# Kernel tuning notes

Hardware: AMD Instinct MI355X
Metric: run time of the kernel (lower is better)

The kernel has to match this reference:

```python
import jax, jax.numpy as jnp
import numpy as np

N = 50000        # nodes
E = 800000       # random edges (plus N self-loops added in setup)
DIN = 128        # input_dim
H = 128          # hidden_dim
L = 3            # num_layers
EPS = 1e-5       # BatchNorm1d eps


def _bn(x, gamma, beta):
    # BatchNorm1d in training mode: batch stats over node axis, biased variance
    m = x.mean(axis=0)
    v = jnp.mean((x - m) ** 2, axis=0)
    return (x - m) * jax.lax.rsqrt(v + EPS) * gamma + beta


def setup_inputs() -> dict:
    key = jax.random.key(0)
    ks = jax.random.split(key, 11)
    feats = jax.random.normal(ks[0], (N, DIN), dtype=jnp.float32)
    # edge list with self-loops so every node has degree >= 1 (average pooling divides by degree)
    loops = jnp.arange(N, dtype=jnp.int64)
    src = jnp.concatenate([jax.random.randint(ks[1], (E,), 0, N, dtype=jnp.int64), loops])
    dst = jnp.concatenate([jax.random.randint(ks[2], (E,), 0, N, dtype=jnp.int64), loops])
    s = 0.05
    # per-layer MLP params (num_mlp_layers=2: Linear -> BN -> ReLU -> Linear), layer 0 has DIN==H
    W1 = jax.random.normal(ks[3], (L, DIN, H), dtype=jnp.float32) * s
    b1 = jnp.zeros((L, H), jnp.float32)
    g1 = jnp.ones((L, H), jnp.float32)
    be1 = jnp.zeros((L, H), jnp.float32)
    W2 = jax.random.normal(ks[4], (L, H, H), dtype=jnp.float32) * s
    b2 = jnp.zeros((L, H), jnp.float32)
    # outer BatchNorm1d per GNN layer
    og = jnp.ones((L, H), jnp.float32)
    ob = jnp.zeros((L, H), jnp.float32)
    return {"feats": feats, "W1": W1, "b1": b1, "g1": g1, "be1": be1,
            "W2": W2, "b2": b2, "og": og, "ob": ob, "src": src, "dst": dst}


def reference(feats, W1, b1, g1, be1, W2, b2, og, ob, src, dst):
    n = feats.shape[0]
    # degree = spmm(Adj, ones) -- constant across layers
    deg = jax.ops.segment_sum(jnp.ones(src.shape, jnp.float32), dst, num_segments=n)[:, None]
    h = feats
    for l in range(L):
        # pooled = spmm(Adj, h) via edge gather + segment reduce, then 'average' normalize
        pooled = jax.ops.segment_sum(h[src], dst, num_segments=n) / deg
        # GIN-style 2-layer MLP: Linear -> BN -> ReLU -> Linear
        z = jax.nn.relu(_bn(pooled @ W1[l] + b1[l], g1[l], be1[l]))
        z = z @ W2[l] + b2[l]
        # outer BatchNorm + ReLU
        h = jax.nn.relu(_bn(z, og[l], ob[l]))
    return h
```

## Files before the change

kernel.cpp:

```cpp
#include <hip/hip_runtime.h>
#include <hip/hip_bf16.h>
#include <stdint.h>

typedef _Float16 h16;
typedef h16 h16x2 __attribute__((ext_vector_type(2)));
typedef h16 h16x8 __attribute__((ext_vector_type(8)));
typedef float f32x4 __attribute__((ext_vector_type(4)));

#define HF 128
#define EPS 1e-5f
#define BSH 9
#define BROWS 512
#define BCAP 16384
#define ECHUNK 8192
#define SBANKS 8

union pk32 { uint32_t u; h16x2 h; };

static __device__ __forceinline__ uint32_t pack_h16(float a, float b) {
    pk32 c;
    c.h[0] = (h16)a; c.h[1] = (h16)b;
    return c.u;
}

static __device__ __forceinline__ float sum8(const float* __restrict__ st, int idx) {
    float s = 0.f;
#pragma unroll
    for (int b = 0; b < SBANKS; b++) s += st[b * 256 + idx];
    return s;
}


__global__ __launch_bounds__(256) void k_bscatter(const int* __restrict__ src,
                                                  const int* __restrict__ dst,
                                                  int* __restrict__ gcursor,
                                                  int2* __restrict__ staging, int ne, int nb) {
    __shared__ int h[128], gb[128];
    const int tid = threadIdx.x;
    if (tid < nb) h[tid] = 0;
    __syncthreads();
    const int beg = blockIdx.x * ECHUNK;
    const int end = min(beg + ECHUNK, ne);
    for (int i = beg + tid; i < end; i += 256)
        atomicAdd(&h[dst[i] >> BSH], 1);
    __syncthreads();
    if (tid < nb) {
        int c = h[tid];
        gb[tid] = c ? atomicAdd(&gcursor[tid], c) : 0;
        h[tid] = 0;
    }
    __syncthreads();
    for (int i = beg + tid; i < end; i += 256) {
        int d = dst[i];
        int b = d >> BSH;
        int r = atomicAdd(&h[b], 1);
        staging[(size_t)b * BCAP + gb[b] + r] = make_int2(src[i], d);
    }
}

__global__ __launch_bounds__(256) void k_bbuild(const int2* __restrict__ staging,
                                                const int* __restrict__ gcursor,
                                                int* __restrict__ rowbeg,
                                                int* __restrict__ rowend,
                                                float* __restrict__ deginv,
                                                int* __restrict__ csrsrc, int n) {
    __shared__ int hist[BROWS];
    __shared__ int scan[BROWS];
    const int b = blockIdx.x;
    const int tid = threadIdx.x;
    const int rb = b << BSH;
    const int nrows = min(BROWS, n - rb);
    const int base = b * BCAP;
    const int cnt = gcursor[b];
    hist[tid] = 0; hist[tid + 256] = 0;
    __syncthreads();
    for (int i = tid; i < cnt; i += 256)
        atomicAdd(&hist[staging[base + i].y - rb], 1);
    __syncthreads();
    const int i0 = tid, i1 = tid + 256;
    scan[i0] = hist[i0]; scan[i1] = hist[i1];
    __syncthreads();
    for (int off = 1; off < BROWS; off <<= 1) {
        int v0 = (i0 >= off) ? scan[i0 - off] : 0;
        int v1 = (i1 >= off) ? scan[i1 - off] : 0;
        __syncthreads();
        scan[i0] += v0; scan[i1] += v1;
        __syncthreads();
    }
    for (int r = tid; r < BROWS; r += 256) {
        int c = hist[r];
        int excl = scan[r] - c;
        if (r < nrows) {
            rowbeg[rb + r] = base + excl;
            rowend[rb + r] = base + excl + c;
            deginv[rb + r] = c ? 1.0f / (float)c : 0.f;
        }
        scan[r] = excl;
    }
    __syncthreads();
    for (int i = tid; i < cnt; i += 256) {
        int2 e = staging[base + i];
        int pos = atomicAdd(&scan[e.y - rb], 1);
        csrsrc[base + pos] = e.x;
    }
}

__global__ __launch_bounds__(256) void k_prep(const float* __restrict__ W1,
                                              const float* __restrict__ W2,
                                              h16* __restrict__ wp,
                                              const float* __restrict__ feats,
                                              uint32_t* __restrict__ hbuf, long tot2) {
    const int bid = (int)blockIdx.x;
    if (bid < 384) {
        const int mat = bid >> 6;
        const int idx = ((bid & 63) << 8) + (int)threadIdx.x;
        const int l = mat >> 1;
        const float* Wsrc = (mat & 1) ? (W2 + l * 16384) : (W1 + l * 16384);
        const int nn = idx >> 7, k = idx & 127;
        float w = Wsrc[k * 128 + nn];
        int pos = nn * 128 + ((((k >> 3) ^ (nn & 7))) << 3) + (k & 7);
        wp[mat * 16384 + pos] = (h16)w;
    } else {
        long i = (long)(bid - 384) * 256 + threadIdx.x;
        if (i < tot2) {
            float2 v = ((const float2*)feats)[i];
            hbuf[i] = pack_h16(v.x, v.y);
        }
    }
}

template <int AFF>
__global__ __launch_bounds__(256) void k_spmm(const uint32_t* __restrict__ hp,
                                              const int* __restrict__ rowbeg,
                                              const int* __restrict__ rowend,
                                              const float* __restrict__ deginv,
                                              const float* __restrict__ st,
                                              const float* __restrict__ g,
                                              const float* __restrict__ be,
                                              float inv_n,
                                              const int* __restrict__ csrsrc,
                                              uint32_t* __restrict__ pooled, int n, int np) {
    const int wid  = (int)((blockIdx.x * 256u + threadIdx.x) >> 6);
    const int lane = threadIdx.x & 63;
    if (wid >= np) return;
    const int gg = lane >> 4;
    const int fl = lane & 15;
    uint4* outrow = (uint4*)(pooled + (size_t)wid * 64);
    if (wid >= n) {
        if (gg == 0) outrow[fl] = make_uint4(0u, 0u, 0u, 0u);
        return;
    }

    uint32_t sv[4], cv[4];
    if (AFF) {
        const int c0 = lane * 2, c1 = c0 + 1;
        float m0 = sum8(st, c0) * inv_n, v0 = sum8(st, 128 + c0) * inv_n - m0 * m0;
        float sx = g[c0] * rsqrtf(v0 + EPS), cx = be[c0] - m0 * sx;
        float m1 = sum8(st, c1) * inv_n, v1 = sum8(st, 128 + c1) * inv_n - m1 * m1;
        float sy = g[c1] * rsqrtf(v1 + EPS), cy = be[c1] - m1 * sy;
        uint32_t su = pack_h16(sx, sy);
        uint32_t cu = pack_h16(cx, cy);
#pragma unroll
        for (int w = 0; w < 4; w++) {
            sv[w] = (uint32_t)__shfl((int)su, fl * 4 + w);
            cv[w] = (uint32_t)__shfl((int)cu, fl * 4 + w);
        }
    }

    const h16 z0 = (h16)0.f;
    h16x2 acc[4];
#pragma unroll
    for (int w = 0; w < 4; w++) acc[w] = (h16x2)z0;

    const int beg = rowbeg[wid], end = rowend[wid];
    for (int base = beg; base < end; base += 64) {
        const int rem = end - base;
        const int cnt = rem < 64 ? rem : 64;
        const int off = lane < cnt ? lane : cnt - 1;
        const int idx = csrsrc[base + off];
        for (int j = 0; j < cnt; j += 32) {
            uint4 p[8];
#pragma unroll
            for (int u = 0; u < 8; u++) {
                const int eb = j + u * 4;
                if (eb < cnt) {
                    int ge = eb + gg;
                    int gec = ge < cnt ? ge : cnt - 1;
                    int s = __shfl(idx, gec);
                    p[u] = *(const uint4*)(hp + (size_t)s * 64 + (fl << 2));
                }
            }
#pragma unroll
            for (int u = 0; u < 8; u++) {
                const int eb = j + u * 4;
                if (eb < cnt) {
                    const uint32_t* pw = (const uint32_t*)&p[u];
                    h16x2 v[4];
#pragma unroll
                    for (int w = 0; w < 4; w++) {
                        pk32 t; t.u = pw[w];
                        h16x2 x = t.h;
                        if (AFF) {
                            pk32 s2; s2.u = sv[w];
                            pk32 c2; c2.u = cv[w];
                            x = x * s2.h + c2.h;
                            x[0] = x[0] > z0 ? x[0] : z0;
                            x[1] = x[1] > z0 ? x[1] : z0;
                        }
                        v[w] = x;
                    }
                    if (eb + gg < cnt) {
#pragma unroll
                        for (int w = 0; w < 4; w++) acc[w] = acc[w] + v[w];
                    }
                }
            }
        }
    }

#pragma unroll
    for (int w = 0; w < 4; w++) {
        pk32 t; t.h = acc[w];
        pk32 r1; r1.u = (uint32_t)__shfl_xor((int)t.u, 16);
        t.h = t.h + r1.h;
        pk32 r2; r2.u = (uint32_t)__shfl_xor((int)t.u, 32);
        t.h = t.h + r2.h;
        acc[w] = t.h;
    }

    const float di = deginv[wid];
    uint4 o;
    o.x = pack_h16((float)acc[0][0] * di, (float)acc[0][1] * di);
    o.y = pack_h16((float)acc[1][0] * di, (float)acc[1][1] * di);
    o.z = pack_h16((float)acc[2][0] * di, (float)acc[2][1] * di);
    o.w = pack_h16((float)acc[3][0] * di, (float)acc[3][1] * di);
    if (gg == 0) outrow[fl] = o;
}

template <int MODE>
__global__ __launch_bounds__(256) void k_gemm(const uint32_t* __restrict__ Ap,
                                              const h16* __restrict__ Wp,
                                              const float* __restrict__ bias,
                                              const float* __restrict__ st,
                                              const float* __restrict__ g,
                                              const float* __restrict__ be,
                                              float inv_n,
                                              h16* __restrict__ Y,
                                              float* __restrict__ outstats, int n) {
    __shared__ __align__(16) h16 WT[128 * 128];
    __shared__ float sred[4][128];
    __shared__ float sred2[4][128];
    __shared__ float aff[256];
    const int tid = threadIdx.x;
    const int wave = tid >> 6, lane = tid & 63;

    {
        const char* gsrc = (const char*)Wp + wave * 1024 + lane * 16;
        char* ldst = (char*)&WT[0] + wave * 1024;
#pragma unroll
        for (int i = 0; i < 8; i++) {
            __builtin_amdgcn_global_load_lds(
                (const __attribute__((address_space(1))) uint32_t*)(gsrc + i * 4096),
                (__attribute__((address_space(3))) uint32_t*)(ldst + i * 4096),
                16, 0, 0);
        }
    }
    if (MODE == 1 && tid < 128) {
        float m = sum8(st, tid) * inv_n;
        float v = sum8(st, 128 + tid) * inv_n - m * m;
        float a = g[tid] * rsqrtf(v + EPS);
        aff[tid] = a;
        aff[128 + tid] = be[tid] - m * a;
    }

    const int lrow = lane & 15, quad = lane >> 4;
    const int bx = (int)blockIdx.x * 128;
    int mb[2];
    mb[0] = bx + wave * 16;
    mb[1] = bx + 64 + wave * 16;

    h16x8 ah[2][4];
    uint4 araw[2][4];
#pragma unroll
    for (int rt = 0; rt < 2; rt++) {
        const uint32_t* arow = Ap + (size_t)(mb[rt] + lrow) * 64 + quad * 4;
#pragma unroll
        for (int kt = 0; kt < 4; kt++)
            araw[rt][kt] = *(const uint4*)(arow + kt * 16);
    }

    __syncthreads();

#pragma unroll
    for (int rt = 0; rt < 2; rt++) {
#pragma unroll
        for (int kt = 0; kt < 4; kt++) {
            if (MODE == 0) {
                ah[rt][kt] = *(const h16x8*)&araw[rt][kt];
            } else {
                const uint32_t* pw = (const uint32_t*)&araw[rt][kt];
                h16x8 t;
#pragma unroll
                for (int j2 = 0; j2 < 4; j2++) {
                    pk32 w; w.u = pw[j2];
                    int k = kt * 32 + quad * 8 + j2 * 2;
                    float x0 = fmaxf(fmaf((float)w.h[0], aff[k],     aff[128 + k]),     0.f);
                    float x1 = fmaxf(fmaf((float)w.h[1], aff[k + 1], aff[129 + k]), 0.f);
                    t[2 * j2]     = (h16)x0;
                    t[2 * j2 + 1] = (h16)x1;
                }
                ah[rt][kt] = t;
            }
        }
    }

    f32x4 acc[2][8];
#pragma unroll
    for (int rt = 0; rt < 2; rt++)
#pragma unroll
        for (int nt = 0; nt < 8; nt++) acc[rt][nt] = (f32x4){0.f, 0.f, 0.f, 0.f};

    const int sw = lrow & 7;
#pragma unroll
    for (int nt = 0; nt < 8; nt++) {
        const h16* wbase = &WT[(nt * 16 + lrow) * 128];
#pragma unroll
        for (int kt = 0; kt < 4; kt++) {
            h16x8 bh = *(const h16x8*)(wbase + (((4 * kt + quad) ^ sw) << 3));
#pragma unroll
            for (int rt = 0; rt < 2; rt++)
                acc[rt][nt] = __builtin_amdgcn_mfma_f32_16x16x32_f16(ah[rt][kt], bh, acc[rt][nt], 0, 0, 0);
        }
    }

#pragma unroll
    for (int nt = 0; nt < 8; nt++) {
        int col = nt * 16 + lrow;
        float bv = bias[col];
        float csum = 0.f, csq = 0.f;
#pragma unroll
        for (int rt = 0; rt < 2; rt++) {
#pragma unroll
            for (int r = 0; r < 4; r++) {
                int row = mb[rt] + quad * 4 + r;
                float yv = acc[rt][nt][r] + bv;
                Y[(size_t)row * 128 + col] = (h16)yv;
                if (row < n) { csum += yv; csq += yv * yv; }
            }
        }
        csum += __shfl_xor(csum, 16, 64); csum += __shfl_xor(csum, 32, 64);
        csq  += __shfl_xor(csq,  16, 64); csq  += __shfl_xor(csq,  32, 64);
        if (quad == 0) { sred[wave][col] = csum; sred2[wave][col] = csq; }
    }
    __syncthreads();
    if (tid < 128) {
        float s = sred[0][tid] + sred[1][tid] + sred[2][tid] + sred[3][tid];
        float q = sred2[0][tid] + sred2[1][tid] + sred2[2][tid] + sred2[3][tid];
        const int bank = (int)(blockIdx.x & (SBANKS - 1));
        atomicAdd(&outstats[bank * 256 + tid], s);
        atomicAdd(&outstats[bank * 256 + 128 + tid], q);
    }
}

__global__ __launch_bounds__(256) void k_bnrelu(const uint32_t* __restrict__ Z,
                                                const float* __restrict__ st,
                                                const float* __restrict__ g,
                                                const float* __restrict__ be,
                                                float inv_n,
                                                float* __restrict__ out, long tot2) {
    long i = (long)blockIdx.x * 256 + threadIdx.x;
    if (i >= tot2) return;
    int c = (int)((i * 2) & 127);
    float m0 = sum8(st, c) * inv_n,     v0 = sum8(st, 128 + c) * inv_n - m0 * m0;
    float a0 = g[c] * rsqrtf(v0 + EPS),     c0 = be[c] - m0 * a0;
    float m1 = sum8(st, c + 1) * inv_n, v1 = sum8(st, 129 + c) * inv_n - m1 * m1;
    float a1 = g[c + 1] * rsqrtf(v1 + EPS), c1 = be[c + 1] - m1 * a1;
    pk32 w; w.u = Z[i];
    float2 o;
    o.x = fmaxf(fmaf((float)w.h[0], a0, c0), 0.f);
    o.y = fmaxf(fmaf((float)w.h[1], a1, c1), 0.f);
    ((float2*)out)[i] = o;
}

extern "C" void kernel_launch(void* const* d_in, const int* in_sizes, int n_in,
                              void* d_out, int out_size, void* d_ws, size_t ws_size,
                              hipStream_t stream) {
    const float* feats = (const float*)d_in[0];
    const float* W1    = (const float*)d_in[1];
    const float* b1    = (const float*)d_in[2];
    const float* g1    = (const float*)d_in[3];
    const float* be1   = (const float*)d_in[4];
    const float* W2    = (const float*)d_in[5];
    const float* b2    = (const float*)d_in[6];
    const float* og    = (const float*)d_in[7];
    const float* ob    = (const float*)d_in[8];
    const int*   src   = (const int*)d_in[9];
    const int*   dst   = (const int*)d_in[10];

    const int n  = in_sizes[0] / HF;
    const int ne = in_sizes[9];
    const int np = (n + 127) & ~127;
    const int nb = (n + BROWS - 1) >> BSH;

    char* p = (char*)d_ws;
    auto alloc = [&](size_t bytes) -> char* {
        char* r = p;
        p += (bytes + 511) & ~(size_t)511;
        return r;
    };
    uint32_t* hbuf    = (uint32_t*)alloc((size_t)np * 64 * 4);
    uint32_t* pooled  = (uint32_t*)alloc((size_t)np * 64 * 4);
    uint32_t* ybuf    = (uint32_t*)alloc((size_t)np * 64 * 4);
    uint32_t* zb      = (uint32_t*)alloc((size_t)np * 64 * 4);
    h16*      wprep   = (h16*)     alloc(6 * 16384 * 2);
    float*    deginv  = (float*)   alloc((size_t)n * 4);
    int*      rowbeg  = (int*)     alloc((size_t)n * 4);
    int*      rowend  = (int*)     alloc((size_t)n * 4);
    int*      csrsrc  = (int*)     alloc((size_t)nb * BCAP * 4);
    int2*     staging = (int2*)    alloc((size_t)nb * BCAP * 8);
    char*     zone    = alloc(512 + 6 * SBANKS * 256 * 4);
    int*      gcursor = (int*)zone;
    float*    stats6  = (float*)(zone + 512);

    hipMemsetAsync(zone, 0, 512 + 6 * SBANKS * 256 * 4, stream);

    const long tot2  = (long)n * (HF / 2);
    const int bnb    = (int)((tot2 + 255) / 256);
    const int spmmb  = np / 4;
    const int gemmb  = np / 128;
    const float inv_n = 1.0f / (float)n;
    const int ebk = (ne + ECHUNK - 1) / ECHUNK;
    const int SL = SBANKS * 256;

    k_prep    <<<384 + bnb, 256, 0, stream>>>(W1, W2, wprep, feats, hbuf, tot2);
    k_bscatter<<<ebk, 256, 0, stream>>>(src, dst, gcursor, staging, ne, nb);
    k_bbuild  <<<nb, 256, 0, stream>>>(staging, gcursor, rowbeg, rowend, deginv, csrsrc, n);

    for (int l = 0; l < 3; l++) {
        float* sY = stats6 + (2 * l) * SL;
        float* sZ = stats6 + (2 * l + 1) * SL;
        if (l == 0)
            k_spmm<0><<<spmmb, 256, 0, stream>>>(hbuf, rowbeg, rowend, deginv,
                                                 nullptr, nullptr, nullptr, inv_n,
                                                 csrsrc, pooled, n, np);
        else
            k_spmm<1><<<spmmb, 256, 0, stream>>>(zb, rowbeg, rowend, deginv,
                                                 stats6 + (2 * (l - 1) + 1) * SL,
                                                 og + (l - 1) * HF, ob + (l - 1) * HF, inv_n,
                                                 csrsrc, pooled, n, np);
        k_gemm<0><<<gemmb, 256, 0, stream>>>(pooled,
                                             wprep + (size_t)(2 * l) * 16384,
                                             b1 + l * HF,
                                             nullptr, nullptr, nullptr, inv_n,
                                             (h16*)ybuf, sY, n);
        k_gemm<1><<<gemmb, 256, 0, stream>>>(ybuf,
                                             wprep + (size_t)(2 * l + 1) * 16384,
                                             b2 + l * HF,
                                             sY, g1 + l * HF, be1 + l * HF, inv_n,
                                             (h16*)zb, sZ, n);
    }
    k_bnrelu<<<bnb, 256, 0, stream>>>(zb, stats6 + 5 * SL, og + 2 * HF, ob + 2 * HF,
                                      inv_n, (float*)d_out, tot2);
}
```

Before: 375.0 us.

## Fuse both MLP GEMMs and final BN-ReLU into one kernel with grid barriers

Merges the two per-layer GEMM kernels into a single kernel that keeps the first GEMM's output tile in LDS. It uses a software grid barrier so the BatchNorm statistics are complete before the second GEMM runs. On the last layer a second barrier lets the kernel apply the outer BN+ReLU directly and write fp32 output, which removes the separate bnrelu kernel. This avoids writing and re-reading the intermediate Y buffer and saves launches. The costs are that all 391 blocks must be co-resident for the barrier to work, and that doubling LDS use for weights can lower occupancy.

Measured after the change: 504.3 us. +34.5%, slower.

```diff
diff --git a/kernel.cpp b/kernel.cpp
--- a/kernel.cpp
+++ b/kernel.cpp
@@ -28,6 +28,26 @@
 #pragma unroll
     for (int b = 0; b < SBANKS; b++) s += st[b * 256 + idx];
     return s;
+}
+
+static __device__ __forceinline__ float sum8c(const float* st, int idx) {
+    float s = 0.f;
+#pragma unroll
+    for (int b = 0; b < SBANKS; b++)
+        s += __hip_atomic_load(&st[b * 256 + idx], __ATOMIC_RELAXED, __HIP_MEMORY_SCOPE_AGENT);
+    return s;
+}
+
+static __device__ __forceinline__ void gridbar(int* ctr, int nblk) {
+    __syncthreads();
+    if (threadIdx.x == 0) {
+        __threadfence();
+        __hip_atomic_fetch_add(ctr, 1, __ATOMIC_ACQ_REL, __HIP_MEMORY_SCOPE_AGENT);
+        while (__hip_atomic_load(ctr, __ATOMIC_ACQUIRE, __HIP_MEMORY_SCOPE_AGENT) < nblk)
+            __builtin_amdgcn_s_sleep(2);
+        __threadfence();
+    }
+    __syncthreads();
 }
 
 
@@ -237,17 +257,25 @@
     if (gg == 0) outrow[fl] = o;
 }
 
-template <int MODE>
-__global__ __launch_bounds__(256) void k_gemm(const uint32_t* __restrict__ Ap,
-                                              const h16* __restrict__ Wp,
-                                              const float* __restrict__ bias,
-                                              const float* __restrict__ st,
-                                              const float* __restrict__ g,
-                                              const float* __restrict__ be,
-                                              float inv_n,
-                                              h16* __restrict__ Y,
-                                              float* __restrict__ outstats, int n) {
-    __shared__ __align__(16) h16 WT[128 * 128];
+template <int LAST>
+__global__ __launch_bounds__(256, 2) void k_fused(const uint32_t* __restrict__ Ap,
+                                                  const h16* __restrict__ Wp1,
+                                                  const h16* __restrict__ Wp2,
+                                                  const float* __restrict__ bias1,
+                                                  const float* __restrict__ bias2,
+                                                  const float* __restrict__ gi,
+                                                  const float* __restrict__ bei,
+                                                  const float* __restrict__ go,
+                                                  const float* __restrict__ bo,
+                                                  float* __restrict__ stY,
+                                                  float* __restrict__ stZ,
+                                                  int* bar1, int* bar2,
+                                                  float inv_n,
+                                                  h16* __restrict__ Zout,
+                                                  float* __restrict__ Fout,
+                                                  int n, int nblk) {
+    __shared__ __align__(16) h16 WT1[128 * 128];
+    __shared__ __align__(16) h16 WT2[128 * 128];
     __shared__ float sred[4][128];
     __shared__ float sred2[4][128];
     __shared__ float aff[256];
@@ -255,35 +283,33 @@
     const int wave = tid >> 6, lane = tid & 63;
 
     {
-        const char* gsrc = (const char*)Wp + wave * 1024 + lane * 16;
-        char* ldst = (char*)&WT[0] + wave * 1024;
+        const char* g1p = (const char*)Wp1 + wave * 1024 + lane * 16;
+        char* l1p = (char*)&WT1[0] + wave * 1024;
+        const char* g2p = (const char*)Wp2 + wave * 1024 + lane * 16;
+        char* l2p = (char*)&WT2[0] + wave * 1024;
 #pragma unroll
         for (int i = 0; i < 8; i++) {
             __builtin_amdgcn_global_load_lds(
-                (const __attribute__((address_space(1))) uint32_t*)(gsrc + i * 4096),
-                (__attribute__((address_space(3))) uint32_t*)(ldst + i * 4096),
+                (const __attribute__((address_space(1))) uint32_t*)(g1p + i * 4096),
+                (__attribute__((address_space(3))) uint32_t*)(l1p + i * 4096),
                 16, 0, 0);
-        }
-    }
-    if (MODE == 1 && tid < 128) {
-        float m = sum8(st, tid) * inv_n;
-        float v = sum8(st, 128 + tid) * inv_n - m * m;
-        float a = g[tid] * rsqrtf(v + EPS);
-        aff[tid] = a;
-        aff[128 + tid] = be[tid] - m * a;
+            __builtin_amdgcn_global_load_lds(
+                (const __attribute__((address_space(1))) uint32_t*)(g2p + i * 4096),
+                (__attribute__((address_space(3))) uint32_t*)(l2p + i * 4096),
+                16, 0, 0);
+        }
     }
 
     const int lrow = lane & 15, quad = lane >> 4;
     const int bx = (int)blockIdx.x * 128;
     int mb[2];
-    mb[0] = bx + wave * 16;
-    mb[1] = bx + 64 + wave * 16;
-
-    h16x8 ah[2][4];
+    mb[0] = wave * 16;
+    mb[1] = 64 + wave * 16;
+
     uint4 araw[2][4];
 #pragma unroll
     for (int rt = 0; rt < 2; rt++) {
-        const uint32_t* arow = Ap + (size_t)(mb[rt] + lrow) * 64 + quad * 4;
+        const uint32_t* arow = Ap + (size_t)(bx + mb[rt] + lrow) * 64 + quad * 4;
 #pragma unroll
         for (int kt = 0; kt < 4; kt++)
             araw[rt][kt] = *(const uint4*)(arow + kt * 16);
@@ -291,29 +317,6 @@
 
     __syncthreads();
 
-#pragma unroll
-    for (int rt = 0; rt < 2; rt++) {
-#pragma unroll
-        for (int kt = 0; kt < 4; kt++) {
-            if (MODE == 0) {
-                ah[rt][kt] = *(const h16x8*)&araw[rt][kt];
-            } else {
-                const uint32_t* pw = (const uint32_t*)&araw[rt][kt];
-                h16x8 t;
-#pragma unroll
-                for (int j2 = 0; j2 < 4; j2++) {
-                    pk32 w; w.u = pw[j2];
-                    int k = kt * 32 + quad * 8 + j2 * 2;
-                    float x0 = fmaxf(fmaf((float)w.h[0], aff[k],     aff[128 + k]),     0.f);
-                    float x1 = fmaxf(fmaf((float)w.h[1], aff[k + 1], aff[129 + k]), 0.f);
-                    t[2 * j2]     = (h16)x0;
-                    t[2 * j2 + 1] = (h16)x1;
-                }
-                ah[rt][kt] = t;
-            }
-        }
-    }
-
     f32x4 acc[2][8];
 #pragma unroll
     for (int rt = 0; rt < 2; rt++)
@@ -323,29 +326,34 @@
     const int sw = lrow & 7;
 #pragma unroll
     for (int nt = 0; nt < 8; nt++) {
-        const h16* wbase = &WT[(nt * 16 + lrow) * 128];
+        const h16* wbase = &WT1[(nt * 16 + lrow) * 128];
 #pragma unroll
         for (int kt = 0; kt < 4; kt++) {
             h16x8 bh = *(const h16x8*)(wbase + (((4 * kt + quad) ^ sw) << 3));
 #pragma unroll
-            for (int rt = 0; rt < 2; rt++)
-                acc[rt][nt] = __builtin_amdgcn_mfma_f32_16x16x32_f16(ah[rt][kt], bh, acc[rt][nt], 0, 0, 0);
-        }
-    }
+            for (int rt = 0; rt < 2; rt++) {
+                h16x8 a = *(const h16x8*)&araw[rt][kt];
+                acc[rt][nt] = __builtin_amdgcn_mfma_f32_16x16x32_f16(a, bh, acc[rt][nt], 0, 0, 0);
+            }
+        }
+    }
+
+    __syncthreads();
 
 #pragma unroll
     for (int nt = 0; nt < 8; nt++) {
         int col = nt * 16 + lrow;
-        float bv = bias[col];
+        float bv = bias1[col];
         float csum = 0.f, csq = 0.f;
 #pragma unroll
         for (int rt = 0; rt < 2; rt++) {
 #pragma unroll
             for (int r = 0; r < 4; r++) {
-                int row = mb[rt] + quad * 4 + r;
+                int rloc = mb[rt] + quad * 4 + r;
                 float yv = acc[rt][nt][r] + bv;
-                Y[(size_t)row * 128 + col] = (h16)yv;
-                if (row < n) { csum += yv; csq += yv * yv; }
+                int byte = rloc * 256 + ((2 * col) ^ ((rloc & 7) << 4));
+                *(h16*)((char*)WT1 + byte) = (h16)yv;
+                if (bx + rloc < n) { csum += yv; csq += yv * yv; }
             }
         }
         csum += __shfl_xor(csum, 16, 64); csum += __shfl_xor(csum, 32, 64);
@@ -357,29 +365,111 @@
         float s = sred[0][tid] + sred[1][tid] + sred[2][tid] + sred[3][tid];
         float q = sred2[0][tid] + sred2[1][tid] + sred2[2][tid] + sred2[3][tid];
         const int bank = (int)(blockIdx.x & (SBANKS - 1));
-        atomicAdd(&outstats[bank * 256 + tid], s);
-        atomicAdd(&outstats[bank * 256 + 128 + tid], q);
-    }
-}
-
-__global__ __launch_bounds__(256) void k_bnrelu(const uint32_t* __restrict__ Z,
-                                                const float* __restrict__ st,
-                                                const float* __restrict__ g,
-                                                const float* __restrict__ be,
-                                                float inv_n,
-                                                float* __restrict__ out, long tot2) {
-    long i = (long)blockIdx.x * 256 + threadIdx.x;
-    if (i >= tot2) return;
-    int c = (int)((i * 2) & 127);
-    float m0 = sum8(st, c) * inv_n,     v0 = sum8(st, 128 + c) * inv_n - m0 * m0;
-    float a0 = g[c] * rsqrtf(v0 + EPS),     c0 = be[c] - m0 * a0;
-    float m1 = sum8(st, c + 1) * inv_n, v1 = sum8(st, 129 + c) * inv_n - m1 * m1;
-    float a1 = g[c + 1] * rsqrtf(v1 + EPS), c1 = be[c + 1] - m1 * a1;
-    pk32 w; w.u = Z[i];
-    float2 o;
-    o.x = fmaxf(fmaf((float)w.h[0], a0, c0), 0.f);
-    o.y = fmaxf(fmaf((float)w.h[1], a1, c1), 0.f);
-    ((float2*)out)[i] = o;
+        atomicAdd(&stY[bank * 256 + tid], s);
+        atomicAdd(&stY[bank * 256 + 128 + tid], q);
+    }
+
+    gridbar(bar1, nblk);
+
+    if (tid < 128) {
+        float m = sum8c(stY, tid) * inv_n;
+        float v = sum8c(stY, 128 + tid) * inv_n - m * m;
+        float a = gi[tid] * rsqrtf(v + EPS);
+        aff[tid] = a;
+        aff[128 + tid] = bei[tid] - m * a;
+    }
+    __syncthreads();
+
+    h16x8 ah2[2][4];
+#pragma unroll
+    for (int rt = 0; rt < 2; rt++) {
+#pragma unroll
+        for (int kt = 0; kt < 4; kt++) {
+            int rloc = mb[rt] + lrow;
+            int byte = rloc * 256 + ((kt * 64 + quad * 16) ^ ((rloc & 7) << 4));
+            h16x8 y8 = *(const h16x8*)((char*)WT1 + byte);
+            int k0 = kt * 32 + quad * 8;
+            h16x8 t;
+#pragma unroll
+            for (int j = 0; j < 8; j++)
+                t[j] = (h16)fmaxf(fmaf((float)y8[j], aff[k0 + j], aff[128 + k0 + j]), 0.f);
+            ah2[rt][kt] = t;
+        }
+    }
+
+    f32x4 acc2[2][8];
+#pragma unroll
+    for (int rt = 0; rt < 2; rt++)
+#pragma unroll
+        for (int nt = 0; nt < 8; nt++) acc2[rt][nt] = (f32x4){0.f, 0.f, 0.f, 0.f};
+
+#pragma unroll
+    for (int nt = 0; nt < 8; nt++) {
+        const h16* wbase = &WT2[(nt * 16 + lrow) * 128];
+#pragma unroll
+        for (int kt = 0; kt < 4; kt++) {
+            h16x8 bh = *(const h16x8*)(wbase + (((4 * kt + quad) ^ sw) << 3));
+#pragma unroll
+            for (int rt = 0; rt < 2; rt++)
+                acc2[rt][nt] = __builtin_amdgcn_mfma_f32_16x16x32_f16(ah2[rt][kt], bh, acc2[rt][nt], 0, 0, 0);
+        }
+    }
+
+#pragma unroll
+    for (int nt = 0; nt < 8; nt++) {
+        int col = nt * 16 + lrow;
+        float bv = bias2[col];
+        float csum = 0.f, csq = 0.f;
+#pragma unroll
+        for (int rt = 0; rt < 2; rt++) {
+#pragma unroll
+            for (int r = 0; r < 4; r++) {
+                int rloc = mb[rt] + quad * 4 + r;
+                int row = bx + rloc;
+                float zv = acc2[rt][nt][r] + bv;
+                acc2[rt][nt][r] = zv;
+                if (!LAST) Zout[(size_t)row * 128 + col] = (h16)zv;
+                if (row < n) { csum += zv; csq += zv * zv; }
+            }
+        }
+        csum += __shfl_xor(csum, 16, 64); csum += __shfl_xor(csum, 32, 64);
+        csq  += __shfl_xor(csq,  16, 64); csq  += __shfl_xor(csq,  32, 64);
+        if (quad == 0) { sred[wave][col] = csum; sred2[wave][col] = csq; }
+    }
+    __syncthreads();
+    if (tid < 128) {
+        float s = sred[0][tid] + sred[1][tid] + sred[2][tid] + sred[3][tid];
+        float q = sred2[0][tid] + sred2[1][tid] + sred2[2][tid] + sred2[3][tid];
+        const int bank = (int)(blockIdx.x & (SBANKS - 1));
+        atomicAdd(&stZ[bank * 256 + tid], s);
+        atomicAdd(&stZ[bank * 256 + 128 + tid], q);
+    }
+
+    if (LAST) {
+        gridbar(bar2, nblk);
+        if (tid < 128) {
+            float m = sum8c(stZ, tid) * inv_n;
+            float v = sum8c(stZ, 128 + tid) * inv_n - m * m;
+            float a = go[tid] * rsqrtf(v + EPS);
+            aff[tid] = a;
+            aff[128 + tid] = bo[tid] - m * a;
+        }
+        __syncthreads();
+#pragma unroll
+        for (int nt = 0; nt < 8; nt++) {
+            int col = nt * 16 + lrow;
+            float a = aff[col], c = aff[128 + col];
+#pragma unroll
+            for (int rt = 0; rt < 2; rt++) {
+#pragma unroll
+                for (int r = 0; r < 4; r++) {
+                    int row = bx + mb[rt] + quad * 4 + r;
+                    if (row < n)
+                        Fout[(size_t)row * 128 + col] = fmaxf(fmaf(acc2[rt][nt][r], a, c), 0.f);
+                }
+            }
+        }
+    }
 }
 
 extern "C" void kernel_launch(void* const* d_in, const int* in_sizes, int n_in,
@@ -410,7 +500,6 @@
     };
     uint32_t* hbuf    = (uint32_t*)alloc((size_t)np * 64 * 4);
     uint32_t* pooled  = (uint32_t*)alloc((size_t)np * 64 * 4);
-    uint32_t* ybuf    = (uint32_t*)alloc((size_t)np * 64 * 4);
     uint32_t* zb      = (uint32_t*)alloc((size_t)np * 64 * 4);
     h16*      wprep   = (h16*)     alloc(6 * 16384 * 2);
     float*    deginv  = (float*)   alloc((size_t)n * 4);
@@ -418,11 +507,12 @@
     int*      rowend  = (int*)     alloc((size_t)n * 4);
     int*      csrsrc  = (int*)     alloc((size_t)nb * BCAP * 4);
     int2*     staging = (int2*)    alloc((size_t)nb * BCAP * 8);
-    char*     zone    = alloc(512 + 6 * SBANKS * 256 * 4);
+    char*     zone    = alloc(1024 + 6 * SBANKS * 256 * 4);
     int*      gcursor = (int*)zone;
-    float*    stats6  = (float*)(zone + 512);
-
-    hipMemsetAsync(zone, 0, 512 + 6 * SBANKS * 256 * 4, stream);
+    int*      bars    = (int*)(zone + 512);
+    float*    stats6  = (float*)(zone + 1024);
+
+    hipMemsetAsync(zone, 0, 1024 + 6 * SBANKS * 256 * 4, stream);
 
     const long tot2  = (long)n * (HF / 2);
     const int bnb    = (int)((tot2 + 255) / 256);
@@ -448,17 +538,25 @@
                                                  stats6 + (2 * (l - 1) + 1) * SL,
                                                  og + (l - 1) * HF, ob + (l - 1) * HF, inv_n,
                                                  csrsrc, pooled, n, np);
-        k_gemm<0><<<gemmb, 256, 0, stream>>>(pooled,
-                                             wprep + (size_t)(2 * l) * 16384,
-                                             b1 + l * HF,
-                                             nullptr, nullptr, nullptr, inv_n,
-                                             (h16*)ybuf, sY, n);
-        k_gemm<1><<<gemmb, 256, 0, stream>>>(ybuf,
-                                             wprep + (size_t)(2 * l + 1) * 16384,
-                                             b2 + l * HF,
-                                             sY, g1 + l * HF, be1 + l * HF, inv_n,
-                                             (h16*)zb, sZ, n);
-    }
-    k_bnrelu<<<bnb, 256, 0, stream>>>(zb, stats6 + 5 * SL, og + 2 * HF, ob + 2 * HF,
-                                      inv_n, (float*)d_out, tot2);
-}
+        if (l < 2)
+            k_fused<0><<<gemmb, 256, 0, stream>>>(pooled,
+                                                  wprep + (size_t)(2 * l) * 16384,
+                                                  wprep + (size_t)(2 * l + 1) * 16384,
+                                                  b1 + l * HF, b2 + l * HF,
+                                                  g1 + l * HF, be1 + l * HF,
+                                                  nullptr, nullptr,
+                                                  sY, sZ,
+                                                  bars + 2 * l, bars + 2 * l + 1,
+                                                  inv_n, (h16*)zb, nullptr, n, gemmb);
+        else
+            k_fused<1><<<gemmb, 256, 0, stream>>>(pooled,
+                                                  wprep + (size_t)(2 * l) * 16384,
+                                                  wprep + (size_t)(2 * l + 1) * 16384,
+                                                  b1 + l * HF, b2 + l * HF,
+                                                  g1 + l * HF, be1 + l * HF,
+                                                  og + 2 * HF, ob + 2 * HF,
+                                                  sY, sZ,
+                                                  bars + 2 * l, bars + 2 * l + 1,
+                                                  inv_n, nullptr, (float*)d_out, n, gemmb);
+    }
+}
```
